# Kernel tuning notes

Hardware: AMD Instinct MI355X
Metric: run time of the kernel (lower is better)

## Reference

```python
import jax, jax.numpy as jnp
import numpy as np

B, T, C = 4, 2048, 1024
H, D = 16, 64  # num_heads, head_dim
P = 64         # prefix length


def setup_inputs() -> dict:
    key = jax.random.key(0)
    ks = jax.random.split(key, 12)
    s = 1.0 / np.sqrt(C)
    return {
        "x": jax.random.normal(ks[0], (B, T, C), dtype=jnp.float32),
        "attn_mask": jax.random.randint(ks[1], (B, 1, 1, T), 0, 2, dtype=jnp.int32),
        "prefix_k": jax.random.normal(ks[2], (B, H, P, D), dtype=jnp.float32),
        "prefix_v": jax.random.normal(ks[3], (B, H, P, D), dtype=jnp.float32),
        "Wq": jax.random.normal(ks[4], (C, C), dtype=jnp.float32) * s,
        "bq": jnp.zeros((C,), dtype=jnp.float32),
        "Wk": jax.random.normal(ks[5], (C, C), dtype=jnp.float32) * s,
        "bk": jnp.zeros((C,), dtype=jnp.float32),
        "Wv": jax.random.normal(ks[6], (C, C), dtype=jnp.float32) * s,
        "bv": jnp.zeros((C,), dtype=jnp.float32),
        "Wo": jax.random.normal(ks[7], (C, C), dtype=jnp.float32) * s,
        "bo": jnp.zeros((C,), dtype=jnp.float32),
    }


def _heads(y):
    # [B,T,C] -> [B,H,T,D]
    return y.reshape(B, T, H, D).transpose(0, 2, 1, 3)


def reference(x, attn_mask, prefix_k, prefix_v, Wq, bq, Wk, bk, Wv, bv, Wo, bo):
    q = _heads(x @ Wq.T + bq)
    k = _heads(x @ Wk.T + bk)
    v = _heads(x @ Wv.T + bv)
    # concat prefix K/V along key dim -> [B,H,P+T,D]
    k = jnp.concatenate([prefix_k, k], axis=2)
    v = jnp.concatenate([prefix_v, v], axis=2)
    # prefix positions are always visible
    prefix_mask = jnp.ones((B, 1, 1, P), dtype=attn_mask.dtype)
    mask = jnp.concatenate([prefix_mask, attn_mask], axis=-1)  # [B,1,1,P+T]
    scores = jnp.einsum('bhtd,bhsd->bhts', q, k) / jnp.sqrt(jnp.asarray(D, x.dtype))
    scores = jnp.where(mask == 0, -jnp.inf, scores)
    w = jax.nn.softmax(scores, axis=-1)
    o = jnp.einsum('bhts,bhsd->bhtd', w, v)
    o = o.transpose(0, 2, 1, 3).reshape(B, T, C)
    return o @ Wo.T + bo
```

## Files before the change

### kernel.cpp

```cpp
#include <hip/hip_runtime.h>
#include <hip/hip_bf16.h>

typedef __bf16 bf16;
typedef __attribute__((ext_vector_type(8))) __bf16 bf16x8;
typedef __attribute__((ext_vector_type(4))) __bf16 bf16x4;
typedef __attribute__((ext_vector_type(4))) float f32x4;
typedef __attribute__((ext_vector_type(16))) float f32x16;

#define MFMA16(a, b, c) __builtin_amdgcn_mfma_f32_16x16x32_bf16(a, b, c, 0, 0, 0)
#define MFMA32(a, b, c) __builtin_amdgcn_mfma_f32_32x32x16_bf16(a, b, c, 0, 0, 0)

__device__ __forceinline__ void gl_lds16(const void* g, void* l) {
    __builtin_amdgcn_global_load_lds(
        (const __attribute__((address_space(1))) void*)g,
        (__attribute__((address_space(3))) void*)l, 16, 0, 0);
}

#define QSCALE 0.18033688011f
#define LOGBIAS 24.0f

__global__ __launch_bounds__(256) void cvt_all(
    const float* __restrict__ x, const float* __restrict__ Wq,
    const float* __restrict__ Wk, const float* __restrict__ Wv,
    const float* __restrict__ Wo, bf16* __restrict__ xb, bf16* __restrict__ wb)
{
    int i4 = blockIdx.x * 256 + threadIdx.x;
    const float* src; bf16* dst; int off;
    if (i4 < 2097152) { src = x; dst = xb; off = i4; }
    else {
        int j = i4 - 2097152;
        int sel = j >> 18;
        off = j & 262143;
        src = (sel == 0) ? Wq : (sel == 1) ? Wk : (sel == 2) ? Wv : Wo;
        dst = wb + (size_t)sel * 1048576;
    }
    float4 a = *(const float4*)&src[(size_t)off * 4];
    bf16x4 o;
    o[0] = (bf16)a.x; o[1] = (bf16)a.y; o[2] = (bf16)a.z; o[3] = (bf16)a.w;
    *(bf16x4*)&dst[(size_t)off * 4] = o;
}

__global__ __launch_bounds__(256) void mask_scan(
    const int* __restrict__ mask, int* __restrict__ slot, int* __restrict__ nk)
{
    const int b = blockIdx.x, tid = threadIdx.x;
    const int lane = tid & 63, wv = tid >> 6;
    const int* mb = mask + b * 2048;
    int loc[8], s = 0;
#pragma unroll
    for (int e = 0; e < 8; ++e) { loc[e] = (mb[tid * 8 + e] != 0); s += loc[e]; }
    int inc = s;
#pragma unroll
    for (int off = 1; off < 64; off <<= 1) {
        int t = __shfl_up(inc, off);
        if (lane >= off) inc += t;
    }
    __shared__ int wt[4];
    if (lane == 63) wt[wv] = inc;
    __syncthreads();
    int wo = 0;
    for (int w = 0; w < wv; ++w) wo += wt[w];
    int excl = wo + inc - s;
#pragma unroll
    for (int e = 0; e < 8; ++e) {
        slot[b * 2048 + tid * 8 + e] = loc[e] ? (64 + excl) : -1;
        excl += loc[e];
    }
    if (tid == 255) nk[b] = 64 + wo + inc;
}

__global__ __launch_bounds__(256) void prefix_cvt(
    const float* __restrict__ pk, const float* __restrict__ pv,
    bf16* __restrict__ k_ws, bf16* __restrict__ vt_ws)
{
    int i = blockIdx.x * 256 + threadIdx.x;
    {
        int base = i * 4;
        int bh = base >> 12, rem = base & 4095;
        float4 a = *(const float4*)&pk[base];
        bf16x4 ab;
        ab[0] = (bf16)a.x; ab[1] = (bf16)a.y; ab[2] = (bf16)a.z; ab[3] = (bf16)a.w;
        *(bf16x4*)&k_ws[(size_t)bh * (2112 * 64) + rem] = ab;
    }
    {
        int bh = i >> 10, r = i & 1023;
        int d = r >> 4, sq = (r & 15) * 4;
        bf16x4 vb;
#pragma unroll
        for (int e = 0; e < 4; ++e)
            vb[e] = (bf16)pv[(size_t)bh * 4096 + (sq + e) * 64 + d];
        *(bf16x4*)&vt_ws[((size_t)bh * 64 + d) * 2112 + sq] = vb;
    }
}

__global__ __launch_bounds__(256) void proj_qkv_gemm(
    const bf16* __restrict__ X, const bf16* __restrict__ Wb,
    const float* __restrict__ bq, const float* __restrict__ bk,
    const float* __restrict__ bv, const int* __restrict__ slot,
    bf16* __restrict__ q_ws, bf16* __restrict__ k_ws, bf16* __restrict__ vt_ws)
{
    __shared__ bf16 As[128 * 32];
    __shared__ bf16 Bs[128 * 32];
    const int mode = blockIdx.z;
    const bf16* __restrict__ W = Wb + (size_t)mode * 1048576;
    const float* __restrict__ bias = (mode == 0) ? bq : (mode == 1) ? bk : bv;
    const int m0 = blockIdx.x * 128, n0 = blockIdx.y * 128;
    const int tid = threadIdx.x, lane = tid & 63, wave = tid >> 6;
    const int ln = lane & 15, quad = lane >> 4;
    const int wr = (wave >> 1) * 64, wc = (wave & 1) * 64;
    const int srow = wave * 32 + (lane >> 2);
    const int scol = (lane & 3) * 8;

    const f32x4 z4 = {0.f, 0.f, 0.f, 0.f};
    f32x4 acc[4][4];
#pragma unroll
    for (int i = 0; i < 4; ++i)
#pragma unroll
        for (int j = 0; j < 4; ++j) acc[i][j] = z4;

    for (int k0 = 0; k0 < 1024; k0 += 32) {
        __syncthreads();
        gl_lds16(&X[(size_t)(m0 + srow) * 1024 + k0 + scol],      &As[(wave * 32) * 32]);
        gl_lds16(&X[(size_t)(m0 + srow + 16) * 1024 + k0 + scol], &As[(wave * 32 + 16) * 32]);
        gl_lds16(&W[(size_t)(n0 + srow) * 1024 + k0 + scol],      &Bs[(wave * 32) * 32]);
        gl_lds16(&W[(size_t)(n0 + srow + 16) * 1024 + k0 + scol], &Bs[(wave * 32 + 16) * 32]);
        __syncthreads();
        bf16x8 af[4], bfr[4];
#pragma unroll
        for (int i = 0; i < 4; ++i) af[i]  = *(const bf16x8*)&As[(wr + i * 16 + ln) * 32 + quad * 8];
#pragma unroll
        for (int j = 0; j < 4; ++j) bfr[j] = *(const bf16x8*)&Bs[(wc + j * 16 + ln) * 32 + quad * 8];
#pragma unroll
        for (int i = 0; i < 4; ++i)
#pragma unroll
            for (int j = 0; j < 4; ++j)
                acc[i][j] = MFMA16(af[i], bfr[j], acc[i][j]);
    }

    if (mode == 0) {
#pragma unroll
        for (int j = 0; j < 4; ++j) {
            const int n = n0 + wc + j * 16 + ln;
            const float bb = bias[n];
            const int h = n >> 6, d = n & 63;
#pragma unroll
            for (int i = 0; i < 4; ++i) {
                int m = m0 + wr + i * 16 + quad * 4;
                int b = m >> 11, t = m & 2047;
#pragma unroll
                for (int r = 0; r < 4; ++r)
                    q_ws[((size_t)(b * 16 + h) * 2048 + t + r) * 64 + d] =
                        (bf16)((acc[i][j][r] + bb) * QSCALE);
            }
        }
    } else {
        int sl[4][4];
        {
            int m = m0 + wr + quad * 4;
            int b = m >> 11;
#pragma unroll
            for (int i = 0; i < 4; ++i) {
                int t = (m + i * 16) & 2047;
#pragma unroll
                for (int r = 0; r < 4; ++r)
                    sl[i][r] = slot[b * 2048 + t + r];
            }
        }
        const int bsel = (m0 + wr) >> 11;
#pragma unroll
        for (int j = 0; j < 4; ++j) {
            const int n = n0 + wc + j * 16 + ln;
            const float bb = bias[n];
            const int h = n >> 6, d = n & 63;
            const size_t bh64 = (size_t)(bsel * 16 + h);
#pragma unroll
            for (int i = 0; i < 4; ++i) {
#pragma unroll
                for (int r = 0; r < 4; ++r) {
                    int s = sl[i][r];
                    if (s >= 0) {
                        bf16 v = (bf16)(acc[i][j][r] + bb);
                        if (mode == 1)
                            k_ws[(bh64 * 2112 + s) * 64 + d] = v;
                        else
                            vt_ws[(bh64 * 64 + d) * 2112 + s] = v;
                    }
                }
            }
        }
    }
}

__global__ __launch_bounds__(256) void attn_kernel(
    const bf16* __restrict__ Q, const bf16* __restrict__ K,
    const bf16* __restrict__ VT, const int* __restrict__ nk,
    bf16* __restrict__ O)
{
    __shared__ bf16 Ks[64 * 72];
    __shared__ bf16 Vt[64 * 72];
    __shared__ bf16 Ps[4][32 * 72];
    const int tid = threadIdx.x, wave = tid >> 6, lane = tid & 63;
    const int ln = lane & 31, hh = lane >> 5;
    const int bh = blockIdx.y, b = bh >> 4, head = bh & 15;
    const bf16* __restrict__ Kb  = K  + (size_t)bh * (2112 * 64);
    const bf16* __restrict__ Vtb = VT + (size_t)bh * (64 * 2112);
    const int qg = blockIdx.x * 128 + wave * 32 + ln;
    const int nkeys = nk[b];
    const int send = ((nkeys + 63) >> 6) << 6;

    bf16x8 qf[4];
#pragma unroll
    for (int kt = 0; kt < 4; ++kt)
        qf[kt] = *(const bf16x8*)&Q[((size_t)bh * 2048 + qg) * 64 + kt * 16 + hh * 8];

    float l_r = 0.f;
    f32x16 acc[2];
#pragma unroll
    for (int r = 0; r < 16; ++r) { acc[0][r] = 0.f; acc[1][r] = 0.f; }

    const int ks_s = tid >> 3, ks_c = (tid & 7) * 8;
    const int vd = tid >> 3,  vs = (tid & 7) * 8;

    bf16x8 kr0, kr1, vr0, vr1;
    kr0 = *(const bf16x8*)&Kb[(size_t)ks_s * 64 + ks_c];
    kr1 = *(const bf16x8*)&Kb[(size_t)(ks_s + 32) * 64 + ks_c];
    vr0 = *(const bf16x8*)&Vtb[(size_t)vd * 2112 + vs];
    vr1 = *(const bf16x8*)&Vtb[(size_t)(vd + 32) * 2112 + vs];

    for (int s0 = 0; s0 < send; s0 += 64) {
        __syncthreads();
        *(bf16x8*)&Ks[ks_s * 72 + ks_c]        = kr0;
        *(bf16x8*)&Ks[(ks_s + 32) * 72 + ks_c] = kr1;
        *(bf16x8*)&Vt[vd * 72 + vs]            = vr0;
        *(bf16x8*)&Vt[(vd + 32) * 72 + vs]     = vr1;
        __syncthreads();

        if (s0 + 64 < send) {
            const int sn = s0 + 64;
            kr0 = *(const bf16x8*)&Kb[(size_t)(sn + ks_s) * 64 + ks_c];
            kr1 = *(const bf16x8*)&Kb[(size_t)(sn + ks_s + 32) * 64 + ks_c];
            vr0 = *(const bf16x8*)&Vtb[(size_t)vd * 2112 + sn + vs];
            vr1 = *(const bf16x8*)&Vtb[(size_t)(vd + 32) * 2112 + sn + vs];
        }

        f32x16 sc[2];
#pragma unroll
        for (int ts = 0; ts < 2; ++ts) {
            f32x16 s16;
#pragma unroll
            for (int r = 0; r < 16; ++r) s16[r] = 0.f;
#pragma unroll
            for (int kt = 0; kt < 4; ++kt) {
                bf16x8 kf = *(const bf16x8*)&Ks[(ts * 32 + ln) * 72 + kt * 16 + hh * 8];
                s16 = MFMA32(kf, qf[kt], s16);
            }
            sc[ts] = s16;
        }

        float rs = 0.f;
        if (s0 + 64 <= nkeys) {
#pragma unroll
            for (int ts = 0; ts < 2; ++ts)
#pragma unroll
                for (int rg = 0; rg < 4; ++rg) {
                    bf16x4 pb;
#pragma unroll
                    for (int i = 0; i < 4; ++i) {
                        float p = __builtin_amdgcn_exp2f(sc[ts][rg * 4 + i] - LOGBIAS);
                        rs += p;
                        pb[i] = (bf16)p;
                    }
                    *(bf16x4*)&Ps[wave][ln * 72 + ts * 32 + rg * 8 + hh * 4] = pb;
                }
        } else {
#pragma unroll
            for (int ts = 0; ts < 2; ++ts)
#pragma unroll
                for (int rg = 0; rg < 4; ++rg) {
                    bf16x4 pb;
#pragma unroll
                    for (int i = 0; i < 4; ++i) {
                        int key = s0 + ts * 32 + rg * 8 + hh * 4 + i;
                        float add = (key < nkeys) ? -LOGBIAS : -1e30f;
                        float p = __builtin_amdgcn_exp2f(sc[ts][rg * 4 + i] + add);
                        rs += p;
                        pb[i] = (bf16)p;
                    }
                    *(bf16x4*)&Ps[wave][ln * 72 + ts * 32 + rg * 8 + hh * 4] = pb;
                }
        }
        l_r += rs;

        __builtin_amdgcn_s_waitcnt(0xC07F);

        bf16x8 pf[4];
#pragma unroll
        for (int ss = 0; ss < 4; ++ss)
            pf[ss] = *(const bf16x8*)&Ps[wave][ln * 72 + ss * 16 + hh * 8];
#pragma unroll
        for (int ss = 0; ss < 4; ++ss) {
            bf16x8 v0 = *(const bf16x8*)&Vt[ln * 72 + ss * 16 + hh * 8];
            acc[0] = MFMA32(v0, pf[ss], acc[0]);
            bf16x8 v1 = *(const bf16x8*)&Vt[(32 + ln) * 72 + ss * 16 + hh * 8];
            acc[1] = MFMA32(v1, pf[ss], acc[1]);
        }
    }

    l_r += __shfl_xor(l_r, 32);
    float inv = 1.0f / l_r;
#pragma unroll
    for (int td = 0; td < 2; ++td)
#pragma unroll
        for (int rg = 0; rg < 4; ++rg) {
            bf16x4 ob;
#pragma unroll
            for (int i = 0; i < 4; ++i) ob[i] = (bf16)(acc[td][rg * 4 + i] * inv);
            *(bf16x4*)&Ps[wave][ln * 72 + td * 32 + rg * 8 + hh * 4] = ob;
        }
    __builtin_amdgcn_s_waitcnt(0xC07F);
    const int orow = lane >> 3, oc = (lane & 7) * 8;
#pragma unroll
    for (int pass = 0; pass < 4; ++pass) {
        int ml = pass * 8 + orow;
        bf16x8 ov = *(const bf16x8*)&Ps[wave][ml * 72 + oc];
        int qrow = blockIdx.x * 128 + wave * 32 + ml;
        *(bf16x8*)&O[((size_t)b * 2048 + qrow) * 1024 + head * 64 + oc] = ov;
    }
}

__global__ __launch_bounds__(256) void out_proj_gemm(
    const bf16* __restrict__ A, const bf16* __restrict__ W,
    const float* __restrict__ bias, float* __restrict__ out)
{
    __shared__ bf16 As[128 * 32];
    __shared__ bf16 Bs[128 * 32];
    const int m0 = blockIdx.x * 128, n0 = blockIdx.y * 128;
    const int tid = threadIdx.x, lane = tid & 63, wave = tid >> 6;
    const int ln = lane & 15, quad = lane >> 4;
    const int wr = (wave >> 1) * 64, wc = (wave & 1) * 64;
    const int srow = wave * 32 + (lane >> 2);
    const int scol = (lane & 3) * 8;

    const f32x4 z4 = {0.f, 0.f, 0.f, 0.f};
    f32x4 acc[4][4];
#pragma unroll
    for (int i = 0; i < 4; ++i)
#pragma unroll
        for (int j = 0; j < 4; ++j) acc[i][j] = z4;

    for (int k0 = 0; k0 < 1024; k0 += 32) {
        __syncthreads();
        gl_lds16(&A[(size_t)(m0 + srow) * 1024 + k0 + scol],      &As[(wave * 32) * 32]);
        gl_lds16(&A[(size_t)(m0 + srow + 16) * 1024 + k0 + scol], &As[(wave * 32 + 16) * 32]);
        gl_lds16(&W[(size_t)(n0 + srow) * 1024 + k0 + scol],      &Bs[(wave * 32) * 32]);
        gl_lds16(&W[(size_t)(n0 + srow + 16) * 1024 + k0 + scol], &Bs[(wave * 32 + 16) * 32]);
        __syncthreads();
        bf16x8 af[4], bfr[4];
#pragma unroll
        for (int i = 0; i < 4; ++i) af[i]  = *(const bf16x8*)&As[(wr + i * 16 + ln) * 32 + quad * 8];
#pragma unroll
        for (int j = 0; j < 4; ++j) bfr[j] = *(const bf16x8*)&Bs[(wc + j * 16 + ln) * 32 + quad * 8];
#pragma unroll
        for (int i = 0; i < 4; ++i)
#pragma unroll
            for (int j = 0; j < 4; ++j)
                acc[i][j] = MFMA16(af[i], bfr[j], acc[i][j]);
    }

#pragma unroll
    for (int j = 0; j < 4; ++j) {
        const int n = n0 + wc + j * 16 + ln;
        const float bb = bias[n];
#pragma unroll
        for (int i = 0; i < 4; ++i) {
#pragma unroll
            for (int r = 0; r < 4; ++r) {
                int m = m0 + wr + i * 16 + quad * 4 + r;
                out[(size_t)m * 1024 + n] = acc[i][j][r] + bb;
            }
        }
    }
}

extern "C" void kernel_launch(void* const* d_in, const int* in_sizes, int n_in,
                              void* d_out, int out_size, void* d_ws, size_t ws_size,
                              hipStream_t stream)
{
    const float* x    = (const float*)d_in[0];
    const int*   mask = (const int*)d_in[1];
    const float* pk   = (const float*)d_in[2];
    const float* pv   = (const float*)d_in[3];
    const float* Wq   = (const float*)d_in[4];
    const float* bq   = (const float*)d_in[5];
    const float* Wk   = (const float*)d_in[6];
    const float* bk   = (const float*)d_in[7];
    const float* Wv   = (const float*)d_in[8];
    const float* bv   = (const float*)d_in[9];
    const float* Wo   = (const float*)d_in[10];
    const float* bo   = (const float*)d_in[11];
    float* out = (float*)d_out;

    bf16* xb    = (bf16*)d_ws;
    bf16* wb    = xb + (size_t)8388608;
    bf16* q_ws  = wb + (size_t)4194304;
    bf16* k_ws  = q_ws + (size_t)8388608;
    bf16* vt_ws = k_ws + (size_t)8650752;
    int*  slot  = (int*)(vt_ws + (size_t)8650752);
    int*  nkv   = slot + 4 * 2048;
    bf16* a_ws  = xb;

    cvt_all<<<dim3(12288), 256, 0, stream>>>(x, Wq, Wk, Wv, Wo, xb, wb);
    mask_scan<<<dim3(4), 256, 0, stream>>>(mask, slot, nkv);
    prefix_cvt<<<dim3(256), 256, 0, stream>>>(pk, pv, k_ws, vt_ws);
    proj_qkv_gemm<<<dim3(64, 8, 3), 256, 0, stream>>>(xb, wb, bq, bk, bv, slot,
                                                      q_ws, k_ws, vt_ws);
    attn_kernel<<<dim3(16, 64), 256, 0, stream>>>(q_ws, k_ws, vt_ws, nkv, a_ws);
    out_proj_gemm<<<dim3(64, 8), 256, 0, stream>>>(a_ws, wb + (size_t)3 * 1048576,
                                                   bo, out);
}
```

Baseline: 283.3 us.

## Compute K/V projections only for unmasked rows via gathered row index

The mask scan now emits a compacted list of visible row indices, and the K/V projection GEMM gathers only those rows of X. Tiles beyond the visible count exit early, which roughly halves K/V GEMM work for a random mask. The three preprocessing kernels are merged into one launch, and the Q projection is split into its own kernel. V stores become vectorised bf16x4 writes. The cost is an indirect row gather in the A-tile loads plus an extra launch for the separate Q GEMM.

```diff
diff --git a/kernel.cpp b/kernel.cpp
--- a/kernel.cpp
+++ b/kernel.cpp
@@ -19,91 +19,83 @@
 #define QSCALE 0.18033688011f
 #define LOGBIAS 24.0f
 
-__global__ __launch_bounds__(256) void cvt_all(
+__global__ __launch_bounds__(256) void prep(
     const float* __restrict__ x, const float* __restrict__ Wq,
     const float* __restrict__ Wk, const float* __restrict__ Wv,
-    const float* __restrict__ Wo, bf16* __restrict__ xb, bf16* __restrict__ wb)
-{
-    int i4 = blockIdx.x * 256 + threadIdx.x;
-    const float* src; bf16* dst; int off;
-    if (i4 < 2097152) { src = x; dst = xb; off = i4; }
-    else {
-        int j = i4 - 2097152;
-        int sel = j >> 18;
-        off = j & 262143;
-        src = (sel == 0) ? Wq : (sel == 1) ? Wk : (sel == 2) ? Wv : Wo;
-        dst = wb + (size_t)sel * 1048576;
-    }
-    float4 a = *(const float4*)&src[(size_t)off * 4];
-    bf16x4 o;
-    o[0] = (bf16)a.x; o[1] = (bf16)a.y; o[2] = (bf16)a.z; o[3] = (bf16)a.w;
-    *(bf16x4*)&dst[(size_t)off * 4] = o;
-}
-
-__global__ __launch_bounds__(256) void mask_scan(
-    const int* __restrict__ mask, int* __restrict__ slot, int* __restrict__ nk)
-{
-    const int b = blockIdx.x, tid = threadIdx.x;
-    const int lane = tid & 63, wv = tid >> 6;
-    const int* mb = mask + b * 2048;
-    int loc[8], s = 0;
-#pragma unroll
-    for (int e = 0; e < 8; ++e) { loc[e] = (mb[tid * 8 + e] != 0); s += loc[e]; }
-    int inc = s;
-#pragma unroll
-    for (int off = 1; off < 64; off <<= 1) {
-        int t = __shfl_up(inc, off);
-        if (lane >= off) inc += t;
-    }
-    __shared__ int wt[4];
-    if (lane == 63) wt[wv] = inc;
-    __syncthreads();
-    int wo = 0;
-    for (int w = 0; w < wv; ++w) wo += wt[w];
-    int excl = wo + inc - s;
-#pragma unroll
-    for (int e = 0; e < 8; ++e) {
-        slot[b * 2048 + tid * 8 + e] = loc[e] ? (64 + excl) : -1;
-        excl += loc[e];
-    }
-    if (tid == 255) nk[b] = 64 + wo + inc;
-}
-
-__global__ __launch_bounds__(256) void prefix_cvt(
-    const float* __restrict__ pk, const float* __restrict__ pv,
-    bf16* __restrict__ k_ws, bf16* __restrict__ vt_ws)
-{
-    int i = blockIdx.x * 256 + threadIdx.x;
-    {
-        int base = i * 4;
-        int bh = base >> 12, rem = base & 4095;
-        float4 a = *(const float4*)&pk[base];
-        bf16x4 ab;
-        ab[0] = (bf16)a.x; ab[1] = (bf16)a.y; ab[2] = (bf16)a.z; ab[3] = (bf16)a.w;
-        *(bf16x4*)&k_ws[(size_t)bh * (2112 * 64) + rem] = ab;
-    }
-    {
-        int bh = i >> 10, r = i & 1023;
-        int d = r >> 4, sq = (r & 15) * 4;
-        bf16x4 vb;
-#pragma unroll
-        for (int e = 0; e < 4; ++e)
-            vb[e] = (bf16)pv[(size_t)bh * 4096 + (sq + e) * 64 + d];
-        *(bf16x4*)&vt_ws[((size_t)bh * 64 + d) * 2112 + sq] = vb;
-    }
-}
-
-__global__ __launch_bounds__(256) void proj_qkv_gemm(
-    const bf16* __restrict__ X, const bf16* __restrict__ Wb,
-    const float* __restrict__ bq, const float* __restrict__ bk,
-    const float* __restrict__ bv, const int* __restrict__ slot,
-    bf16* __restrict__ q_ws, bf16* __restrict__ k_ws, bf16* __restrict__ vt_ws)
+    const float* __restrict__ Wo, const float* __restrict__ pk,
+    const float* __restrict__ pv, const int* __restrict__ mask,
+    bf16* __restrict__ xb, bf16* __restrict__ wb,
+    bf16* __restrict__ k_ws, bf16* __restrict__ vt_ws,
+    int* __restrict__ ridx, int* __restrict__ nkv)
+{
+    const int blk = blockIdx.x, tid = threadIdx.x;
+    if (blk < 4) {
+        const int b = blk, lane = tid & 63, wv = tid >> 6;
+        const int* mb = mask + b * 2048;
+        int loc[8], s = 0;
+#pragma unroll
+        for (int e = 0; e < 8; ++e) { loc[e] = (mb[tid * 8 + e] != 0); s += loc[e]; }
+        int inc = s;
+#pragma unroll
+        for (int off = 1; off < 64; off <<= 1) {
+            int t = __shfl_up(inc, off);
+            if (lane >= off) inc += t;
+        }
+        __shared__ int wt[4];
+        if (lane == 63) wt[wv] = inc;
+        __syncthreads();
+        int wo = 0;
+        for (int w = 0; w < wv; ++w) wo += wt[w];
+        int excl = wo + inc - s;
+#pragma unroll
+        for (int e = 0; e < 8; ++e) {
+            if (loc[e]) ridx[b * 2048 + excl] = tid * 8 + e;
+            excl += loc[e];
+        }
+        if (tid == 255) nkv[b] = 64 + wo + inc;
+    } else if (blk < 260) {
+        int i = (blk - 4) * 256 + tid;
+        {
+            int base = i * 4;
+            int bh = base >> 12, rem = base & 4095;
+            float4 a = *(const float4*)&pk[base];
+            bf16x4 ab;
+            ab[0] = (bf16)a.x; ab[1] = (bf16)a.y; ab[2] = (bf16)a.z; ab[3] = (bf16)a.w;
+            *(bf16x4*)&k_ws[(size_t)bh * (2112 * 64) + rem] = ab;
+        }
+        {
+            int bh = i >> 10, r = i & 1023;
+            int d = r >> 4, sq = (r & 15) * 4;
+            bf16x4 vb;
+#pragma unroll
+            for (int e = 0; e < 4; ++e)
+                vb[e] = (bf16)pv[(size_t)bh * 4096 + (sq + e) * 64 + d];
+            *(bf16x4*)&vt_ws[((size_t)bh * 64 + d) * 2112 + sq] = vb;
+        }
+    } else {
+        int i4 = (blk - 260) * 256 + tid;
+        const float* src; bf16* dst; int off;
+        if (i4 < 2097152) { src = x; dst = xb; off = i4; }
+        else {
+            int j = i4 - 2097152;
+            int sel = j >> 18;
+            off = j & 262143;
+            src = (sel == 0) ? Wq : (sel == 1) ? Wk : (sel == 2) ? Wv : Wo;
+            dst = wb + (size_t)sel * 1048576;
+        }
+        float4 a = *(const float4*)&src[(size_t)off * 4];
+        bf16x4 o;
+        o[0] = (bf16)a.x; o[1] = (bf16)a.y; o[2] = (bf16)a.z; o[3] = (bf16)a.w;
+        *(bf16x4*)&dst[(size_t)off * 4] = o;
+    }
+}
+
+__global__ __launch_bounds__(256) void proj_q_gemm(
+    const bf16* __restrict__ X, const bf16* __restrict__ W,
+    const float* __restrict__ bias, bf16* __restrict__ q_ws)
 {
     __shared__ bf16 As[128 * 32];
     __shared__ bf16 Bs[128 * 32];
-    const int mode = blockIdx.z;
-    const bf16* __restrict__ W = Wb + (size_t)mode * 1048576;
-    const float* __restrict__ bias = (mode == 0) ? bq : (mode == 1) ? bk : bv;
     const int m0 = blockIdx.x * 128, n0 = blockIdx.y * 128;
     const int tid = threadIdx.x, lane = tid & 63, wave = tid >> 6;
     const int ln = lane & 15, quad = lane >> 4;
@@ -137,54 +129,105 @@
                 acc[i][j] = MFMA16(af[i], bfr[j], acc[i][j]);
     }
 
-    if (mode == 0) {
-#pragma unroll
-        for (int j = 0; j < 4; ++j) {
-            const int n = n0 + wc + j * 16 + ln;
-            const float bb = bias[n];
-            const int h = n >> 6, d = n & 63;
-#pragma unroll
-            for (int i = 0; i < 4; ++i) {
-                int m = m0 + wr + i * 16 + quad * 4;
-                int b = m >> 11, t = m & 2047;
+#pragma unroll
+    for (int j = 0; j < 4; ++j) {
+        const int n = n0 + wc + j * 16 + ln;
+        const float bb = bias[n];
+        const int h = n >> 6, d = n & 63;
+#pragma unroll
+        for (int i = 0; i < 4; ++i) {
+            int m = m0 + wr + i * 16 + quad * 4;
+            int b = m >> 11, t = m & 2047;
+#pragma unroll
+            for (int r = 0; r < 4; ++r)
+                q_ws[((size_t)(b * 16 + h) * 2048 + t + r) * 64 + d] =
+                    (bf16)((acc[i][j][r] + bb) * QSCALE);
+        }
+    }
+}
+
+__global__ __launch_bounds__(256) void proj_kv_gemm(
+    const bf16* __restrict__ X, const bf16* __restrict__ Wb,
+    const float* __restrict__ bk, const float* __restrict__ bv,
+    const int* __restrict__ ridx, const int* __restrict__ nkv,
+    bf16* __restrict__ k_ws, bf16* __restrict__ vt_ws)
+{
+    const int bsel = blockIdx.x >> 4, tile = blockIdx.x & 15;
+    const int nvis = nkv[bsel] - 64;
+    const int mbase = tile * 128;
+    if (mbase >= nvis) return;
+
+    __shared__ bf16 As[128 * 32];
+    __shared__ bf16 Bs[128 * 32];
+    const int mode = blockIdx.z;
+    const bf16* __restrict__ W = Wb + (size_t)(1 + mode) * 1048576;
+    const float* __restrict__ bias = mode ? bv : bk;
+    const int n0 = blockIdx.y * 128;
+    const int tid = threadIdx.x, lane = tid & 63, wave = tid >> 6;
+    const int ln = lane & 15, quad = lane >> 4;
+    const int wr = (wave >> 1) * 64, wc = (wave & 1) * 64;
+    const int srow = wave * 32 + (lane >> 2);
+    const int scol = (lane & 3) * 8;
+
+    int g0 = mbase + srow,      g1 = g0 + 16;
+    int c0 = (g0 < nvis) ? g0 : nvis - 1;
+    int c1 = (g1 < nvis) ? g1 : nvis - 1;
+    const bf16* Xr0 = X + (size_t)(bsel * 2048 + ridx[bsel * 2048 + c0]) * 1024 + scol;
+    const bf16* Xr1 = X + (size_t)(bsel * 2048 + ridx[bsel * 2048 + c1]) * 1024 + scol;
+
+    const f32x4 z4 = {0.f, 0.f, 0.f, 0.f};
+    f32x4 acc[4][4];
+#pragma unroll
+    for (int i = 0; i < 4; ++i)
+#pragma unroll
+        for (int j = 0; j < 4; ++j) acc[i][j] = z4;
+
+    for (int k0 = 0; k0 < 1024; k0 += 32) {
+        __syncthreads();
+        gl_lds16(Xr0 + k0, &As[(wave * 32) * 32]);
+        gl_lds16(Xr1 + k0, &As[(wave * 32 + 16) * 32]);
+        gl_lds16(&W[(size_t)(n0 + srow) * 1024 + k0 + scol],      &Bs[(wave * 32) * 32]);
+        gl_lds16(&W[(size_t)(n0 + srow + 16) * 1024 + k0 + scol], &Bs[(wave * 32 + 16) * 32]);
+        __syncthreads();
+        bf16x8 af[4], bfr[4];
+#pragma unroll
+        for (int i = 0; i < 4; ++i) af[i]  = *(const bf16x8*)&As[(wr + i * 16 + ln) * 32 + quad * 8];
+#pragma unroll
+        for (int j = 0; j < 4; ++j) bfr[j] = *(const bf16x8*)&Bs[(wc + j * 16 + ln) * 32 + quad * 8];
+#pragma unroll
+        for (int i = 0; i < 4; ++i)
+#pragma unroll
+            for (int j = 0; j < 4; ++j)
+                acc[i][j] = MFMA16(af[i], bfr[j], acc[i][j]);
+    }
+
+#pragma unroll
+    for (int j = 0; j < 4; ++j) {
+        const int n = n0 + wc + j * 16 + ln;
+        const float bb = bias[n];
+        const int h = n >> 6, d = n & 63;
+        const size_t bh64 = (size_t)(bsel * 16 + h);
+#pragma unroll
+        for (int i = 0; i < 4; ++i) {
+            int ml = mbase + wr + i * 16 + quad * 4;
+            if (mode == 0) {
 #pragma unroll
                 for (int r = 0; r < 4; ++r)
-                    q_ws[((size_t)(b * 16 + h) * 2048 + t + r) * 64 + d] =
-                        (bf16)((acc[i][j][r] + bb) * QSCALE);
-            }
-        }
-    } else {
-        int sl[4][4];
-        {
-            int m = m0 + wr + quad * 4;
-            int b = m >> 11;
-#pragma unroll
-            for (int i = 0; i < 4; ++i) {
-                int t = (m + i * 16) & 2047;
-#pragma unroll
-                for (int r = 0; r < 4; ++r)
-                    sl[i][r] = slot[b * 2048 + t + r];
-            }
-        }
-        const int bsel = (m0 + wr) >> 11;
-#pragma unroll
-        for (int j = 0; j < 4; ++j) {
-            const int n = n0 + wc + j * 16 + ln;
-            const float bb = bias[n];
-            const int h = n >> 6, d = n & 63;
-            const size_t bh64 = (size_t)(bsel * 16 + h);
-#pragma unroll
-            for (int i = 0; i < 4; ++i) {
-#pragma unroll
-                for (int r = 0; r < 4; ++r) {
-                    int s = sl[i][r];
-                    if (s >= 0) {
-                        bf16 v = (bf16)(acc[i][j][r] + bb);
-                        if (mode == 1)
-                            k_ws[(bh64 * 2112 + s) * 64 + d] = v;
-                        else
-                            vt_ws[(bh64 * 64 + d) * 2112 + s] = v;
-                    }
+                    if (ml + r < nvis)
+                        k_ws[(bh64 * 2112 + 64 + ml + r) * 64 + d] =
+                            (bf16)(acc[i][j][r] + bb);
+            } else {
+                if (ml + 3 < nvis) {
+                    bf16x4 pb;
+#pragma unroll
+                    for (int r = 0; r < 4; ++r) pb[r] = (bf16)(acc[i][j][r] + bb);
+                    *(bf16x4*)&vt_ws[(bh64 * 64 + d) * 2112 + 64 + ml] = pb;
+                } else {
+#pragma unroll
+                    for (int r = 0; r < 4; ++r)
+                        if (ml + r < nvis)
+                            vt_ws[(bh64 * 64 + d) * 2112 + 64 + ml + r] =
+                                (bf16)(acc[i][j][r] + bb);
                 }
             }
         }
@@ -405,15 +448,15 @@
     bf16* q_ws  = wb + (size_t)4194304;
     bf16* k_ws  = q_ws + (size_t)8388608;
     bf16* vt_ws = k_ws + (size_t)8650752;
-    int*  slot  = (int*)(vt_ws + (size_t)8650752);
-    int*  nkv   = slot + 4 * 2048;
+    int*  ridx  = (int*)(vt_ws + (size_t)8650752);
+    int*  nkv   = ridx + 4 * 2048;
     bf16* a_ws  = xb;
 
-    cvt_all<<<dim3(12288), 256, 0, stream>>>(x, Wq, Wk, Wv, Wo, xb, wb);
-    mask_scan<<<dim3(4), 256, 0, stream>>>(mask, slot, nkv);
-    prefix_cvt<<<dim3(256), 256, 0, stream>>>(pk, pv, k_ws, vt_ws);
-    proj_qkv_gemm<<<dim3(64, 8, 3), 256, 0, stream>>>(xb, wb, bq, bk, bv, slot,
-                                                      q_ws, k_ws, vt_ws);
+    prep<<<dim3(12548), 256, 0, stream>>>(x, Wq, Wk, Wv, Wo, pk, pv, mask,
+                                          xb, wb, k_ws, vt_ws, ridx, nkv);
+    proj_q_gemm<<<dim3(64, 8), 256, 0, stream>>>(xb, wb, bq, q_ws);
+    proj_kv_gemm<<<dim3(64, 8, 2), 256, 0, stream>>>(xb, wb, bk, bv, ridx, nkv,
+                                                     k_ws, vt_ws);
     attn_kernel<<<dim3(16, 64), 256, 0, stream>>>(q_ws, k_ws, vt_ws, nkv, a_ws);
     out_proj_gemm<<<dim3(64, 8), 256, 0, stream>>>(a_ws, wb + (size_t)3 * 1048576,
                                                    bo, out);
```

Result: faster. 275.3 us (-2.8%).
